# Kernel tuning notes

Measured on AMD Instinct MI355X. Metric: run time of the kernel, lower is better.

Reference implementation:

```python
import jax, jax.numpy as jnp
import numpy as np

EMBED_DIM = 512
NUM_HEADS = 8
HEAD_DIM = EMBED_DIM // NUM_HEADS
GRID_SHAPE = (48, 48)
WINDOW = (16, 16)
BATCH = 2
SEQ = GRID_SHAPE[0] * GRID_SHAPE[1]
NEG = float(np.finfo(np.float16).min)  # matches torch.finfo(torch.float16).min fill


def build_window_mask():
    # replicates: indices = np.indices(grid).flatten(1).T; dist = |i-j|*2; all(dist < window)
    idx = np.indices(GRID_SHAPE).reshape(len(GRID_SHAPE), -1).T  # [N, 2]
    dist = np.abs(idx[:, None, :] - idx[None, :, :]) * 2          # [N, N, 2]
    mask = np.all(dist < np.array(WINDOW)[None, None, :], axis=-1)  # [N, N] bool
    return jnp.asarray(mask)


def setup_inputs() -> dict:
    key = jax.random.key(0)
    ks = jax.random.split(key, 11)
    s = 1.0 / np.sqrt(EMBED_DIM)
    inp = {
        "x_q": jax.random.normal(ks[0], (BATCH, SEQ, EMBED_DIM), jnp.float32),
        "x_k": jax.random.normal(ks[1], (BATCH, SEQ, EMBED_DIM), jnp.float32),
        "x_v": jax.random.normal(ks[2], (BATCH, SEQ, EMBED_DIM), jnp.float32),
        "Wq": jax.random.normal(ks[3], (EMBED_DIM, EMBED_DIM), jnp.float32) * s,
        "bq": jnp.zeros((EMBED_DIM,), jnp.float32),
        "Wk": jax.random.normal(ks[4], (EMBED_DIM, EMBED_DIM), jnp.float32) * s,
        "bk": jnp.zeros((EMBED_DIM,), jnp.float32),
        "Wv": jax.random.normal(ks[5], (EMBED_DIM, EMBED_DIM), jnp.float32) * s,
        "bv": jnp.zeros((EMBED_DIM,), jnp.float32),
        "Wo": jax.random.normal(ks[6], (EMBED_DIM, EMBED_DIM), jnp.float32) * s,
        "bo": jnp.zeros((EMBED_DIM,), jnp.float32),
        "attn_mask": build_window_mask(),
    }
    return inp


def reference(x_q, x_k, x_v, Wq, bq, Wk, bk, Wv, bv, Wo, bo, attn_mask):
    B, S, E = x_q.shape
    H, D = NUM_HEADS, HEAD_DIM

    def proj(x, W, b):
        y = x @ W.T + b                         # [B,S,E]
        return y.reshape(B, S, H, D).transpose(0, 2, 1, 3)  # [B,H,S,D]

    q = proj(x_q, Wq, bq)
    k = proj(x_k, Wk, bk)
    v = proj(x_v, Wv, bv)

    scores = jnp.einsum("bhqd,bhkd->bhqk", q, k) / np.sqrt(D)
    # Windowed branch: per-row gather over allowed keys + softmax == dense
    # softmax with disallowed keys masked to a huge negative value.
    scores = jnp.where(attn_mask[None, None, :, :], scores, NEG)
    probs = jax.nn.softmax(scores, axis=-1)     # dropout=0.0 -> identity
    context = jnp.einsum("bhqk,bhkd->bhqd", probs, v)
    context = context.transpose(0, 2, 1, 3).reshape(B, S, E)
    out = context @ Wo.T + bo
    return out
```

## Files before the change

### kernel.cpp

```cpp
#include <hip/hip_runtime.h>

typedef __attribute__((ext_vector_type(8))) short short8;
typedef __attribute__((ext_vector_type(4))) float f32x4;
typedef __attribute__((ext_vector_type(2))) unsigned int u32x2;
typedef __attribute__((ext_vector_type(4))) unsigned int u32x4;

#define DEV __device__ __forceinline__

#define QH_E 0L
#define KH_E 2359296L
#define VT_E 4718592L
#define CTX_E 7077888L

#define LOG2E 1.4426950408889634f

#define BARRIER() __builtin_amdgcn_s_barrier()
#define SCHED0() __builtin_amdgcn_sched_barrier(0)

DEV unsigned short f2bf(float f) {
  unsigned int x = __float_as_uint(f);
  x = (x + 0x7fffu + ((x >> 16) & 1u)) >> 16;
  return (unsigned short)x;
}

DEV unsigned int pk2(float a, float b) {
  unsigned int r;
  asm("v_cvt_pk_bf16_f32 %0, %1, %2" : "=v"(r) : "v"(a), "v"(b));
  return r;
}

DEV void gl2lds16(const unsigned short* g, unsigned short* l) {
  __builtin_amdgcn_global_load_lds(
      (const __attribute__((address_space(1))) unsigned int*)g,
      (__attribute__((address_space(3))) unsigned int*)l, 16, 0, 0);
}

DEV f32x4 mfma16(short8 a, short8 b, f32x4 c) {
  return __builtin_amdgcn_mfma_f32_16x16x32_bf16(a, b, c, 0, 0, 0);
}

DEV void gemm_qkv(const float* __restrict__ A, const float* __restrict__ W,
                  int m0, int n0, unsigned short* ldsA, unsigned short* ldsB,
                  f32x4 acc[4][2]) {
  const int tid = threadIdx.x;
  const int lane = tid & 63, wvv = tid >> 6;
  const int g = lane >> 4, qi = lane & 15;
  const int wr = wvv >> 1, wc = wvv & 1;
  const int c8 = tid & 7, rbase = tid >> 3;
  const int j8 = (c8 ^ (rbase & 7)) * 8;
  f32x4 ra[4][2];
  f32x4 rw[2][2][2];
#pragma unroll
  for (int mi = 0; mi < 4; ++mi)
#pragma unroll
    for (int ni = 0; ni < 2; ++ni) {
      f32x4 z = {0.f, 0.f, 0.f, 0.f};
      acc[mi][ni] = z;
    }
#define QLA(kt) do {                                                          \
    const int k0_ = (kt) * 64;                                                \
    _Pragma("unroll")                                                         \
    for (int it = 0; it < 4; ++it) {                                          \
      const float* p = A + (long)(m0 + it * 32 + rbase) * 512 + k0_ + j8;     \
      ra[it][0] = *(const f32x4*)p;                                           \
      ra[it][1] = *(const f32x4*)(p + 4);                                     \
    }                                                                         \
  } while (0)
#define QLB(kt) do {                                                          \
    const int k0_ = (kt) * 64;                                                \
    _Pragma("unroll")                                                         \
    for (int it = 0; it < 2; ++it) {                                          \
      const float* p = W + (long)(n0 + it * 32 + rbase) * 512 + k0_ + j8;     \
      rw[(kt) & 1][it][0] = *(const f32x4*)p;                                 \
      rw[(kt) & 1][it][1] = *(const f32x4*)(p + 4);                           \
    }                                                                         \
  } while (0)
#define QWA(bi) do {                                                          \
    _Pragma("unroll")                                                         \
    for (int it = 0; it < 4; ++it) {                                          \
      u32x4 v_;                                                               \
      v_.x = pk2(ra[it][0].x, ra[it][0].y);                                   \
      v_.y = pk2(ra[it][0].z, ra[it][0].w);                                   \
      v_.z = pk2(ra[it][1].x, ra[it][1].y);                                   \
      v_.w = pk2(ra[it][1].z, ra[it][1].w);                                   \
      *(u32x4*)(ldsA + (bi) * 8192 + (it * 256 + tid) * 8) = v_;              \
    }                                                                         \
  } while (0)
#define QWB(bi) do {                                                          \
    _Pragma("unroll")                                                         \
    for (int it = 0; it < 2; ++it) {                                          \
      u32x4 v_;                                                               \
      v_.x = pk2(rw[(bi)][it][0].x, rw[(bi)][it][0].y);                       \
      v_.y = pk2(rw[(bi)][it][0].z, rw[(bi)][it][0].w);                       \
      v_.z = pk2(rw[(bi)][it][1].x, rw[(bi)][it][1].y);                       \
      v_.w = pk2(rw[(bi)][it][1].z, rw[(bi)][it][1].w);                       \
      *(u32x4*)(ldsB + (bi) * 4096 + (it * 256 + tid) * 8) = v_;              \
    }                                                                         \
  } while (0)
  QLA(0); QLB(0); QLB(1);
  QWA(0); QWB(0);
  QLA(1); QLB(2);
  asm volatile("s_waitcnt lgkmcnt(0)" ::: "memory");
  BARRIER();
  SCHED0();
#pragma unroll
  for (int kt = 0; kt < 8; ++kt) {
    const unsigned short* La = ldsA + (kt & 1) * 8192;
    const unsigned short* Lb = ldsB + (kt & 1) * 4096;
    __builtin_amdgcn_s_setprio(1);
#pragma unroll
    for (int kk = 0; kk < 2; ++kk) {
      short8 af[4], bfr[2];
#pragma unroll
      for (int mi = 0; mi < 4; ++mi) {
        int row = 64 * wr + 16 * mi + qi;
        int c16 = (4 * kk + g) ^ (qi & 7);
        af[mi] = *(const short8*)(La + row * 64 + c16 * 8);
      }
#pragma unroll
      for (int ni = 0; ni < 2; ++ni) {
        int row = 32 * wc + 16 * ni + qi;
        int c16 = (4 * kk + g) ^ (qi & 7);
        bfr[ni] = *(const short8*)(Lb + row * 64 + c16 * 8);
      }
#pragma unroll
      for (int mi = 0; mi < 4; ++mi)
#pragma unroll
        for (int ni = 0; ni < 2; ++ni)
          acc[mi][ni] = mfma16(af[mi], bfr[ni], acc[mi][ni]);
    }
    __builtin_amdgcn_s_setprio(0);
    SCHED0();
    if (kt < 7) { QWA((kt + 1) & 1); QWB((kt + 1) & 1); }
    if (kt < 6) QLA(kt + 2);
    if (kt < 5) QLB(kt + 3);
    if (kt < 7) {
      asm volatile("s_waitcnt lgkmcnt(0)" ::: "memory");
      BARRIER();
      SCHED0();
    }
  }
#undef QLA
#undef QLB
#undef QWA
#undef QWB
}

DEV void gemm_o(const unsigned short* __restrict__ A, const float* __restrict__ W,
                int m0, int n0, unsigned short* ldsA, unsigned short* ldsB,
                f32x4 acc[2][2]) {
  const int tid = threadIdx.x;
  const int lane = tid & 63, wvv = tid >> 6;
  const int g = lane >> 4, qi = lane & 15;
  const int wr = wvv >> 1, wc = wvv & 1;
  const int c8 = tid & 7, rbase = tid >> 3;
  const int j8 = (c8 ^ (rbase & 7)) * 8;
  u32x4 rab[2][2];
  f32x4 rw[2][2][2];
#pragma unroll
  for (int mi = 0; mi < 2; ++mi)
#pragma unroll
    for (int ni = 0; ni < 2; ++ni) {
      f32x4 z = {0.f, 0.f, 0.f, 0.f};
      acc[mi][ni] = z;
    }
#define OLA(kt) do {                                                          \
    const int k0_ = (kt) * 64;                                                \
    _Pragma("unroll")                                                         \
    for (int it = 0; it < 2; ++it)                                            \
      rab[(kt) & 1][it] =                                                     \
          *(const u32x4*)(A + (long)(m0 + it * 32 + rbase) * 512 + k0_ + j8); \
  } while (0)
#define OLB(kt) do {                                                          \
    const int k0_ = (kt) * 64;                                                \
    _Pragma("unroll")                                                         \
    for (int it = 0; it < 2; ++it) {                                          \
      const float* p = W + (long)(n0 + it * 32 + rbase) * 512 + k0_ + j8;     \
      rw[(kt) & 1][it][0] = *(const f32x4*)p;                                 \
// ... 33 lines not shown
    for (int kk = 0; kk < 2; ++kk) {
      short8 af[2], bfr[2];
#pragma unroll
      for (int mi = 0; mi < 2; ++mi) {
        int row = 32 * wr + 16 * mi + qi;
        int c16 = (4 * kk + g) ^ (qi & 7);
        af[mi] = *(const short8*)(La + row * 64 + c16 * 8);
      }
#pragma unroll
      for (int ni = 0; ni < 2; ++ni) {
        int row = 32 * wc + 16 * ni + qi;
        int c16 = (4 * kk + g) ^ (qi & 7);
        bfr[ni] = *(const short8*)(Lb + row * 64 + c16 * 8);
      }
#pragma unroll
      for (int mi = 0; mi < 2; ++mi)
#pragma unroll
        for (int ni = 0; ni < 2; ++ni)
          acc[mi][ni] = mfma16(af[mi], bfr[ni], acc[mi][ni]);
    }
    __builtin_amdgcn_s_setprio(0);
    SCHED0();
    if (kt < 6) OW(kt + 2);
    if (kt < 4) { OLA(kt + 4); OLB(kt + 4); }
    if (kt < 7) {
      asm volatile("s_waitcnt lgkmcnt(0)" ::: "memory");
      BARRIER();
      SCHED0();
    }
  }
#undef OLA
#undef OLB
#undef OW
}

__global__ __launch_bounds__(256, 3) void proj_qkv_kernel(
    const float* __restrict__ xq, const float* __restrict__ xk,
    const float* __restrict__ xv, const float* __restrict__ wqp,
    const float* __restrict__ wkp, const float* __restrict__ wvp,
    const float* __restrict__ bq, const float* __restrict__ bk,
    const float* __restrict__ bv, unsigned short* __restrict__ ws) {
  __shared__ unsigned short ldsA[2 * 8192];
  __shared__ unsigned short ldsB[2 * 4096];
  int f = blockIdx.x;
  int wid = (f & 7) * 108 + (f >> 3);
  const int z = wid / 288;
  const int rem = wid % 288;
  const int m0 = (rem >> 3) * 128, n0 = (rem & 7) * 64;
  const float *A, *W, *bias;
  unsigned short* dst;
  float oscale;
  int mode;
  if (z == 0)      { A = xq; W = wqp; bias = bq; oscale = 0.125f * LOG2E; dst = ws + QH_E; mode = 0; }
  else if (z == 1) { A = xk; W = wkp; bias = bk; oscale = 1.0f;           dst = ws + KH_E; mode = 0; }
  else             { A = xv; W = wvp; bias = bv; oscale = 1.0f;           dst = ws + VT_E; mode = 1; }
  f32x4 acc[4][2];
  gemm_qkv(A, W, m0, n0, ldsA, ldsB, acc);
  const int lane = threadIdx.x & 63, wvv = threadIdx.x >> 6;
  const int g = lane >> 4, qi = lane & 15;
  const int wr = wvv >> 1, wc = wvv & 1;
#pragma unroll
  for (int ni = 0; ni < 2; ++ni) {
    int n = n0 + 32 * wc + 16 * ni + qi;
    float bb = bias[n];
    int h = n >> 6, d = n & 63;
#pragma unroll
    for (int mi = 0; mi < 4; ++mi) {
      int m = m0 + 64 * wr + 16 * mi + 4 * g;
      int b = (m >= 2304) ? 1 : 0;
      int s = m - b * 2304;
      if (mode == 0) {
#pragma unroll
        for (int r = 0; r < 4; ++r) {
          float v = (acc[mi][ni][r] + bb) * oscale;
          dst[((long)((b * 8 + h) * 2304 + s + r)) * 64 + d] = f2bf(v);
        }
      } else {
        u32x2 o;
        o.x = pk2(acc[mi][ni][0] + bb, acc[mi][ni][1] + bb);
        o.y = pk2(acc[mi][ni][2] + bb, acc[mi][ni][3] + bb);
        *(u32x2*)(dst + ((long)((b * 8 + h) * 64 + d)) * 2304 + s) = o;
      }
    }
  }
}

__global__ __launch_bounds__(256, 3) void proj_out_kernel(
    const unsigned short* __restrict__ ws, const float* __restrict__ wop,
    const float* __restrict__ bo, float* __restrict__ out) {
  __shared__ unsigned short ldsA[3 * 4096];
  __shared__ unsigned short ldsB[3 * 4096];
  int f = blockIdx.x;
  int wid = (f & 7) * 72 + (f >> 3);
  const int m0 = (wid >> 3) * 64, n0 = (wid & 7) * 64;
  f32x4 acc[2][2];
  gemm_o(ws + CTX_E, wop, m0, n0, ldsA, ldsB, acc);
  const int lane = threadIdx.x & 63, wvv = threadIdx.x >> 6;
  const int g = lane >> 4, qi = lane & 15;
  const int wr = wvv >> 1, wc = wvv & 1;
#pragma unroll
  for (int ni = 0; ni < 2; ++ni) {
    int n = n0 + 32 * wc + 16 * ni + qi;
    float bb = bo[n];
#pragma unroll
    for (int mi = 0; mi < 2; ++mi) {
#pragma unroll
      for (int r = 0; r < 4; ++r) {
        int m = m0 + 32 * wr + 16 * mi + 4 * g + r;
        out[(long)m * 512 + n] = acc[mi][ni][r] + bb;
      }
    }
  }
}

__global__ __launch_bounds__(192) void attn_kernel(unsigned short* __restrict__ ws) {
  __shared__ unsigned short ldsKV[3 * 7168];
  __shared__ unsigned short ldsP[3][16][72];
  __shared__ unsigned short ldsDum[512];
  const int tid = threadIdx.x;
  const int lane = tid & 63, wv = tid >> 6;
  const int g = lane >> 4, qi = lane & 15;
  int f = blockIdx.x;
  int wid = (f & 7) * 96 + (f >> 3);
  const int bh = wid / 48, r = wid - 48 * bh;
  const int ci = wv * 16 + qi;
  const unsigned short* Kh = ws + KH_E + (long)bh * 2304 * 64;
  const unsigned short* Vt = ws + VT_E + (long)bh * 64 * 2304;
  const int q = r * 48 + ci;
  const unsigned short* qp = ws + QH_E + ((long)bh * 2304 + q) * 64;
  f32x4 qraw0 = *(const f32x4*)(qp + 8 * g);
  f32x4 qraw1 = *(const f32x4*)(qp + 32 + 8 * g);
  asm volatile("" : "+v"(qraw0), "+v"(qraw1));
  short8 qf0 = __builtin_bit_cast(short8, qraw0);
  short8 qf1 = __builtin_bit_cast(short8, qraw1);
  float msk[12];
#pragma unroll
  for (int mb = 0; mb < 3; ++mb)
#pragma unroll
    for (int rr = 0; rr < 4; ++rr) {
      int cj = 16 * mb + 4 * g + rr;
      msk[mb * 4 + rr] = ((unsigned)(ci - cj + 7) <= 14u) ? 0.f : -1e30f;
    }
  {
    u32x2 z2; z2.x = 0u; z2.y = 0u;
    *(u32x2*)(&ldsP[wv][qi][48 + 4 * g]) = z2;
  }
  f32x4 cacc[4];
#pragma unroll
  for (int mb = 0; mb < 4; ++mb) { f32x4 z = {0.f, 0.f, 0.f, 0.f}; cacc[mb] = z; }
  float lrun = 0.f;

#define ASTAGE(bi, rj) do {                                                   \
    unsigned short* Lb_ = ldsKV + (bi) * 7168;                                \
    const unsigned short* Ks_ = Kh + (long)(rj) * 3072;                       \
    _Pragma("unroll")                                                         \
    for (int it = 0; it < 5; ++it) {                                          \
      int u = it * 192 + tid;                                                 \
      if (u < 384) {                                                          \
        int kr = u >> 3, c = u & 7, cs = c ^ (kr & 7);                        \
        gl2lds16(Ks_ + kr * 64 + cs * 8, Lb_ + u * 8);                        \
      } else if (u < 896) {                                                   \
        int v2 = u - 384;                                                     \
        int d = v2 >> 3, c = v2 & 7, cs = c ^ (d & 7);                        \
        long jb = (long)(rj) * 48 + cs * 8;                                   \
        if (jb > 2296) jb = 2296;                                             \
        gl2lds16(Vt + (long)d * 2304 + jb, Lb_ + u * 8);                      \
      } else {                                                                \
        gl2lds16(Kh + (u - 896) * 8, ldsDum + (u - 896) * 8);                 \
      }                                                                       \
    }                                                                         \
  } while (0)

  const int rlo = (r > 7) ? r - 7 : 0;
  const int rhi = (r < 40) ? r + 7 : 47;
  const int nch = rhi - rlo + 1;
  ASTAGE(0, rlo);
  ASTAGE(1, rlo + 1);
  for (int t = 0; t < nch; ++t) {
    if (t + 1 < nch) { asm volatile("s_waitcnt vmcnt(5)" ::: "memory"); }
    else             { asm volatile("s_waitcnt vmcnt(0)" ::: "memory"); }
    BARRIER();
    SCHED0();
    if (t + 2 < nch) ASTAGE((t + 2) % 3, rlo + t + 2);
    const unsigned short* Kt = ldsKV + (t % 3) * 7168;
    const unsigned short* Vm = Kt + 3072;
    f32x4 sacc[3];
#pragma unroll
    for (int mb = 0; mb < 3; ++mb) { f32x4 z = {0.f, 0.f, 0.f, 0.f}; sacc[mb] = z; }
    __builtin_amdgcn_s_setprio(1);
#pragma unroll
    for (int kk = 0; kk < 2; ++kk) {
      short8 qf = kk ? qf1 : qf0;
#pragma unroll
      for (int mb = 0; mb < 3; ++mb) {
        int row = 16 * mb + qi;
        int c16 = (4 * kk + g) ^ (qi & 7);
        short8 ka = *(const short8*)(Kt + row * 64 + c16 * 8);
        sacc[mb] = mfma16(ka, qf, sacc[mb]);
      }
    }
    __builtin_amdgcn_s_setprio(0);
    unsigned int pw[6];
#pragma unroll
    for (int mb = 0; mb < 3; ++mb) {
      float p0 = __builtin_amdgcn_exp2f(sacc[mb][0] + msk[mb * 4 + 0]);
      float p1 = __builtin_amdgcn_exp2f(sacc[mb][1] + msk[mb * 4 + 1]);
      float p2 = __builtin_amdgcn_exp2f(sacc[mb][2] + msk[mb * 4 + 2]);
      float p3 = __builtin_amdgcn_exp2f(sacc[mb][3] + msk[mb * 4 + 3]);
      lrun += (p0 + p1) + (p2 + p3);
      pw[2 * mb] = pk2(p0, p1);
      pw[2 * mb + 1] = pk2(p2, p3);
    }
#pragma unroll
    for (int mb = 0; mb < 3; ++mb) {
      u32x2 pv2; pv2.x = pw[2 * mb]; pv2.y = pw[2 * mb + 1];
      *(u32x2*)(&ldsP[wv][qi][16 * mb + 4 * g]) = pv2;
    }
    __builtin_amdgcn_s_setprio(1);
#pragma unroll
    for (int kk = 0; kk < 2; ++kk) {
      short8 pb = *(const short8*)(&ldsP[wv][qi][32 * kk + 8 * g]);
#pragma unroll
      for (int mb = 0; mb < 4; ++mb) {
        int row = 16 * mb + qi;
        int c16 = (4 * kk + g) ^ (qi & 7);
        short8 va = *(const short8*)(Vm + row * 64 + c16 * 8);
        cacc[mb] = mfma16(va, pb, cacc[mb]);
      }
    }
    __builtin_amdgcn_s_setprio(0);
  }
#undef ASTAGE
  lrun += __shfl_xor(lrun, 16);
  lrun += __shfl_xor(lrun, 32);
  const float inv = 1.0f / lrun;
  unsigned short* ctx = ws + CTX_E;
  const int b2 = bh >> 3, h2 = bh & 7;
#pragma unroll
  for (int mb = 0; mb < 4; ++mb) {
    u32x2 o;
    o.x = pk2(cacc[mb][0] * inv, cacc[mb][1] * inv);
    o.y = pk2(cacc[mb][2] * inv, cacc[mb][3] * inv);
    long off = ((long)(b2 * 2304 + q)) * 512 + h2 * 64 + 16 * mb + 4 * g;
    *(u32x2*)(ctx + off) = o;
  }
}

extern "C" void kernel_launch(void* const* d_in, const int* in_sizes, int n_in,
                              void* d_out, int out_size, void* d_ws, size_t ws_size,
                              hipStream_t stream) {
  const float* xq = (const float*)d_in[0];
  const float* xk = (const float*)d_in[1];
  const float* xv = (const float*)d_in[2];
  const float* wq = (const float*)d_in[3];
  const float* bq = (const float*)d_in[4];
  const float* wk = (const float*)d_in[5];
  const float* bk = (const float*)d_in[6];
  const float* wv = (const float*)d_in[7];
  const float* bv = (const float*)d_in[8];
  const float* wo = (const float*)d_in[9];
  const float* bo = (const float*)d_in[10];
  unsigned short* ws = (unsigned short*)d_ws;
  float* out = (float*)d_out;

  proj_qkv_kernel<<<dim3(864), dim3(256), 0, stream>>>(xq, xk, xv, wq, wk, wv,
                                                       bq, bk, bv, ws);
  attn_kernel<<<dim3(768), dim3(192), 0, stream>>>(ws);
  proj_out_kernel<<<dim3(576), dim3(256), 0, stream>>>(ws, wo, bo, out);
}
```

Measured before the change: 57.49 us.

## Software-pipeline QK of next chunk with softmax-PV of current chunk

Restructures the windowed attention loop so the QK^T MFMAs for chunk t+1 are issued before the exp/softmax and PV MFMAs of chunk t, using two ping-pong score register sets and a manually unrolled by-two loop. The aim is to overlap the matrix-core work with the transcendental and LDS work so dependent latencies are hidden. The trade-off is more live registers, a stricter vmcnt(0) wait before each stage where the old code used vmcnt(5), and more complex buffer rotation. This could reduce occupancy or expose load latency.

New measurement: 57.90 us. No clear change (+0.7%).

```diff
diff --git a/kernel.cpp b/kernel.cpp
--- a/kernel.cpp
+++ b/kernel.cpp
@@ -382,77 +382,102 @@
     }                                                                         \
   } while (0)
 
+#define AQK(KB, S) do {                                                       \
+    const unsigned short* Kt_ = (KB);                                         \
+    _Pragma("unroll")                                                         \
+    for (int mb = 0; mb < 3; ++mb) { f32x4 z = {0.f,0.f,0.f,0.f}; S[mb] = z; }\
+    __builtin_amdgcn_s_setprio(1);                                            \
+    _Pragma("unroll")                                                         \
+    for (int kk = 0; kk < 2; ++kk) {                                          \
+      short8 qf_ = kk ? qf1 : qf0;                                            \
+      _Pragma("unroll")                                                       \
+      for (int mb = 0; mb < 3; ++mb) {                                        \
+        int row = 16 * mb + qi;                                               \
+        int c16 = (4 * kk + g) ^ (qi & 7);                                    \
+        short8 ka = *(const short8*)(Kt_ + row * 64 + c16 * 8);               \
+        S[mb] = mfma16(ka, qf_, S[mb]);                                       \
+      }                                                                       \
+    }                                                                         \
+    __builtin_amdgcn_s_setprio(0);                                            \
+  } while (0)
+
+#define ASMPV(VB, S) do {                                                     \
+    const unsigned short* Vm_ = (VB);                                         \
+    unsigned int pw[6];                                                       \
+    _Pragma("unroll")                                                         \
+    for (int mb = 0; mb < 3; ++mb) {                                          \
+      float p0 = __builtin_amdgcn_exp2f(S[mb][0] + msk[mb * 4 + 0]);          \
+      float p1 = __builtin_amdgcn_exp2f(S[mb][1] + msk[mb * 4 + 1]);          \
+      float p2 = __builtin_amdgcn_exp2f(S[mb][2] + msk[mb * 4 + 2]);          \
+      float p3 = __builtin_amdgcn_exp2f(S[mb][3] + msk[mb * 4 + 3]);          \
+      lrun += (p0 + p1) + (p2 + p3);                                          \
+      pw[2 * mb] = pk2(p0, p1);                                               \
+      pw[2 * mb + 1] = pk2(p2, p3);                                           \
+    }                                                                         \
+    _Pragma("unroll")                                                         \
+    for (int mb = 0; mb < 3; ++mb) {                                          \
+      u32x2 pv2; pv2.x = pw[2 * mb]; pv2.y = pw[2 * mb + 1];                  \
+      *(u32x2*)(&ldsP[wv][qi][16 * mb + 4 * g]) = pv2;                        \
+    }                                                                         \
+    __builtin_amdgcn_s_setprio(1);                                            \
+    _Pragma("unroll")                                                         \
+    for (int kk = 0; kk < 2; ++kk) {                                          \
+      short8 pb = *(const short8*)(&ldsP[wv][qi][32 * kk + 8 * g]);           \
+      _Pragma("unroll")                                                       \
+      for (int mb = 0; mb < 4; ++mb) {                                        \
+        int row = 16 * mb + qi;                                               \
+        int c16 = (4 * kk + g) ^ (qi & 7);                                    \
+        short8 va = *(const short8*)(Vm_ + row * 64 + c16 * 8);               \
+        cacc[mb] = mfma16(va, pb, cacc[mb]);                                  \
+      }                                                                       \
+    }                                                                         \
+    __builtin_amdgcn_s_setprio(0);                                            \
+  } while (0)
+
   const int rlo = (r > 7) ? r - 7 : 0;
   const int rhi = (r < 40) ? r + 7 : 47;
   const int nch = rhi - rlo + 1;
+  f32x4 sE[3], sO[3];
   ASTAGE(0, rlo);
   ASTAGE(1, rlo + 1);
-  for (int t = 0; t < nch; ++t) {
-    if (t + 1 < nch) { asm volatile("s_waitcnt vmcnt(5)" ::: "memory"); }
-    else             { asm volatile("s_waitcnt vmcnt(0)" ::: "memory"); }
+  asm volatile("s_waitcnt vmcnt(5)" ::: "memory");
+  BARRIER();
+  SCHED0();
+  AQK(ldsKV, sE);
+  int bc = 0;
+  for (int t = 0; t < nch; t += 2) {
+    const int b1 = (bc + 1 == 3) ? 0 : bc + 1;
+    const int b2 = (b1 + 1 == 3) ? 0 : b1 + 1;
+    asm volatile("s_waitcnt vmcnt(0)" ::: "memory");
     BARRIER();
     SCHED0();
-    if (t + 2 < nch) ASTAGE((t + 2) % 3, rlo + t + 2);
-    const unsigned short* Kt = ldsKV + (t % 3) * 7168;
-    const unsigned short* Vm = Kt + 3072;
-    f32x4 sacc[3];
-#pragma unroll
-    for (int mb = 0; mb < 3; ++mb) { f32x4 z = {0.f, 0.f, 0.f, 0.f}; sacc[mb] = z; }
-    __builtin_amdgcn_s_setprio(1);
-#pragma unroll
-    for (int kk = 0; kk < 2; ++kk) {
-      short8 qf = kk ? qf1 : qf0;
-#pragma unroll
-      for (int mb = 0; mb < 3; ++mb) {
-        int row = 16 * mb + qi;
-        int c16 = (4 * kk + g) ^ (qi & 7);
-        short8 ka = *(const short8*)(Kt + row * 64 + c16 * 8);
-        sacc[mb] = mfma16(ka, qf, sacc[mb]);
-      }
-    }
-    __builtin_amdgcn_s_setprio(0);
-    unsigned int pw[6];
-#pragma unroll
-    for (int mb = 0; mb < 3; ++mb) {
-      float p0 = __builtin_amdgcn_exp2f(sacc[mb][0] + msk[mb * 4 + 0]);
-      float p1 = __builtin_amdgcn_exp2f(sacc[mb][1] + msk[mb * 4 + 1]);
-      float p2 = __builtin_amdgcn_exp2f(sacc[mb][2] + msk[mb * 4 + 2]);
-      float p3 = __builtin_amdgcn_exp2f(sacc[mb][3] + msk[mb * 4 + 3]);
-      lrun += (p0 + p1) + (p2 + p3);
-      pw[2 * mb] = pk2(p0, p1);
-      pw[2 * mb + 1] = pk2(p2, p3);
-    }
-#pragma unroll
-    for (int mb = 0; mb < 3; ++mb) {
-      u32x2 pv2; pv2.x = pw[2 * mb]; pv2.y = pw[2 * mb + 1];
-      *(u32x2*)(&ldsP[wv][qi][16 * mb + 4 * g]) = pv2;
-    }
-    __builtin_amdgcn_s_setprio(1);
-#pragma unroll
-    for (int kk = 0; kk < 2; ++kk) {
-      short8 pb = *(const short8*)(&ldsP[wv][qi][32 * kk + 8 * g]);
-#pragma unroll
-      for (int mb = 0; mb < 4; ++mb) {
-        int row = 16 * mb + qi;
-        int c16 = (4 * kk + g) ^ (qi & 7);
-        short8 va = *(const short8*)(Vm + row * 64 + c16 * 8);
-        cacc[mb] = mfma16(va, pb, cacc[mb]);
-      }
-    }
-    __builtin_amdgcn_s_setprio(0);
+    if (t + 2 < nch) ASTAGE(b2, rlo + t + 2);
+    if (t + 1 < nch) AQK(ldsKV + b1 * 7168, sO);
+    ASMPV(ldsKV + bc * 7168 + 3072, sE);
+    if (t + 1 < nch) {
+      asm volatile("s_waitcnt vmcnt(0)" ::: "memory");
+      BARRIER();
+      SCHED0();
+      if (t + 3 < nch) ASTAGE(bc, rlo + t + 3);
+      if (t + 2 < nch) AQK(ldsKV + b2 * 7168, sE);
+      ASMPV(ldsKV + b1 * 7168 + 3072, sO);
+    }
+    bc = b2;
   }
 #undef ASTAGE
+#undef AQK
+#undef ASMPV
   lrun += __shfl_xor(lrun, 16);
   lrun += __shfl_xor(lrun, 32);
   const float inv = 1.0f / lrun;
   unsigned short* ctx = ws + CTX_E;
-  const int b2 = bh >> 3, h2 = bh & 7;
+  const int b2w = bh >> 3, h2 = bh & 7;
 #pragma unroll
   for (int mb = 0; mb < 4; ++mb) {
     u32x2 o;
     o.x = pk2(cacc[mb][0] * inv, cacc[mb][1] * inv);
     o.y = pk2(cacc[mb][2] * inv, cacc[mb][3] * inv);
-    long off = ((long)(b2 * 2304 + q)) * 512 + h2 * 64 + 16 * mb + 4 * g;
+    long off = ((long)(b2w * 2304 + q)) * 512 + h2 * 64 + 16 * mb + 4 * g;
     *(u32x2*)(ctx + off) = o;
   }
 }
```

## Enlarge QKV projection tiles and share K/V staging across two query rows

Applied to the files above, without the earlier changes.

The QKV projection kernel now uses 512-thread blocks with 128x128 output tiles instead of 256-thread 128x64 tiles, halving the block count and raising reuse of each loaded A tile. The attention kernel now processes two adjacent query grid rows per 384-thread block, so each staged K/V row chunk in LDS serves both rows. Chunks outside a row's window are skipped per wave. This cuts redundant global K/V traffic, but gives fewer blocks, a larger LDS footprint and some idle waves at window edges.

Measured after the change: 61.67 us. +7.3%, slower.

```diff
diff --git a/kernel.cpp b/kernel.cpp
--- a/kernel.cpp
+++ b/kernel.cpp
@@ -39,74 +39,94 @@
   return __builtin_amdgcn_mfma_f32_16x16x32_bf16(a, b, c, 0, 0, 0);
 }
 
-DEV void gemm_qkv(const float* __restrict__ A, const float* __restrict__ W,
-                  int m0, int n0, unsigned short* ldsA, unsigned short* ldsB,
-                  f32x4 acc[4][2]) {
+__global__ __launch_bounds__(512, 4) void proj_qkv_kernel(
+    const float* __restrict__ xq, const float* __restrict__ xk,
+    const float* __restrict__ xv, const float* __restrict__ wqp,
+    const float* __restrict__ wkp, const float* __restrict__ wvp,
+    const float* __restrict__ bq, const float* __restrict__ bk,
+    const float* __restrict__ bv, unsigned short* __restrict__ ws) {
+  __shared__ unsigned short ldsA[2 * 8192];
+  __shared__ unsigned short ldsB[2 * 8192];
+  int f = blockIdx.x;
+  int wid = (f & 7) * 54 + (f >> 3);
+  const int z = wid / 144;
+  const int rem = wid % 144;
+  const int m0 = (rem >> 2) * 128, n0 = (rem & 3) * 128;
+  const float *A, *W, *bias;
+  unsigned short* dst;
+  float oscale;
+  int mode;
+  if (z == 0)      { A = xq; W = wqp; bias = bq; oscale = 0.125f * LOG2E; dst = ws + QH_E; mode = 0; }
+  else if (z == 1) { A = xk; W = wkp; bias = bk; oscale = 1.0f;           dst = ws + KH_E; mode = 0; }
+  else             { A = xv; W = wvp; bias = bv; oscale = 1.0f;           dst = ws + VT_E; mode = 1; }
   const int tid = threadIdx.x;
   const int lane = tid & 63, wvv = tid >> 6;
   const int g = lane >> 4, qi = lane & 15;
-  const int wr = wvv >> 1, wc = wvv & 1;
+  const int wr = wvv >> 2, wc = wvv & 3;
   const int c8 = tid & 7, rbase = tid >> 3;
-  const int j8 = (c8 ^ (rbase & 7)) * 8;
-  f32x4 ra[4][2];
-  f32x4 rw[2][2][2];
+  f32x4 ra[2][2], rw[2][2];
+  f32x4 acc[4][2];
 #pragma unroll
   for (int mi = 0; mi < 4; ++mi)
 #pragma unroll
     for (int ni = 0; ni < 2; ++ni) {
-      f32x4 z = {0.f, 0.f, 0.f, 0.f};
-      acc[mi][ni] = z;
-    }
-#define QLA(kt) do {                                                          \
+      f32x4 z4 = {0.f, 0.f, 0.f, 0.f};
+      acc[mi][ni] = z4;
+    }
+#define PLA(kt) do {                                                          \
     const int k0_ = (kt) * 64;                                                \
     _Pragma("unroll")                                                         \
-    for (int it = 0; it < 4; ++it) {                                          \
-      const float* p = A + (long)(m0 + it * 32 + rbase) * 512 + k0_ + j8;     \
+    for (int it = 0; it < 2; ++it) {                                          \
+      int row = it * 64 + rbase;                                              \
+      int cs = c8 ^ (row & 7);                                                \
+      const float* p = A + (long)(m0 + row) * 512 + k0_ + cs * 8;             \
       ra[it][0] = *(const f32x4*)p;                                           \
       ra[it][1] = *(const f32x4*)(p + 4);                                     \
     }                                                                         \
   } while (0)
-#define QLB(kt) do {                                                          \
+#define PLB(kt) do {                                                          \
     const int k0_ = (kt) * 64;                                                \
     _Pragma("unroll")                                                         \
     for (int it = 0; it < 2; ++it) {                                          \
-      const float* p = W + (long)(n0 + it * 32 + rbase) * 512 + k0_ + j8;     \
-      rw[(kt) & 1][it][0] = *(const f32x4*)p;                                 \
-      rw[(kt) & 1][it][1] = *(const f32x4*)(p + 4);                           \
-    }                                                                         \
-  } while (0)
-#define QWA(bi) do {                                                          \
-    _Pragma("unroll")                                                         \
-    for (int it = 0; it < 4; ++it) {                                          \
+      int row = it * 64 + rbase;                                              \
+      int cs = c8 ^ (row & 7);                                                \
+      const float* p = W + (long)(n0 + row) * 512 + k0_ + cs * 8;             \
+      rw[it][0] = *(const f32x4*)p;                                           \
+      rw[it][1] = *(const f32x4*)(p + 4);                                     \
+    }                                                                         \
+  } while (0)
+#define PWA(bi) do {                                                          \
+    _Pragma("unroll")                                                         \
+    for (int it = 0; it < 2; ++it) {                                          \
       u32x4 v_;                                                               \
       v_.x = pk2(ra[it][0].x, ra[it][0].y);                                   \
       v_.y = pk2(ra[it][0].z, ra[it][0].w);                                   \
       v_.z = pk2(ra[it][1].x, ra[it][1].y);                                   \
       v_.w = pk2(ra[it][1].z, ra[it][1].w);                                   \
-      *(u32x4*)(ldsA + (bi) * 8192 + (it * 256 + tid) * 8) = v_;              \
-    }                                                                         \
-  } while (0)
-#define QWB(bi) do {                                                          \
+      *(u32x4*)(ldsA + (bi) * 8192 + (it * 512 + tid) * 8) = v_;              \
+    }                                                                         \
+  } while (0)
+#define PWB(bi) do {                                                          \
     _Pragma("unroll")                                                         \
     for (int it = 0; it < 2; ++it) {                                          \
       u32x4 v_;                                                               \
-      v_.x = pk2(rw[(bi)][it][0].x, rw[(bi)][it][0].y);                       \
-      v_.y = pk2(rw[(bi)][it][0].z, rw[(bi)][it][0].w);                       \
-      v_.z = pk2(rw[(bi)][it][1].x, rw[(bi)][it][1].y);                       \
-      v_.w = pk2(rw[(bi)][it][1].z, rw[(bi)][it][1].w);                       \
-      *(u32x4*)(ldsB + (bi) * 4096 + (it * 256 + tid) * 8) = v_;              \
-    }                                                                         \
-  } while (0)
-  QLA(0); QLB(0); QLB(1);
-  QWA(0); QWB(0);
-  QLA(1); QLB(2);
+      v_.x = pk2(rw[it][0].x, rw[it][0].y);                                   \
+      v_.y = pk2(rw[it][0].z, rw[it][0].w);                                   \
+      v_.z = pk2(rw[it][1].x, rw[it][1].y);                                   \
+      v_.w = pk2(rw[it][1].z, rw[it][1].w);                                   \
+      *(u32x4*)(ldsB + (bi) * 8192 + (it * 512 + tid) * 8) = v_;              \
+    }                                                                         \
+  } while (0)
+  PLA(0); PLB(0);
+  PWA(0); PWB(0);
+  PLA(1); PLB(1);
   asm volatile("s_waitcnt lgkmcnt(0)" ::: "memory");
   BARRIER();
   SCHED0();
 #pragma unroll
   for (int kt = 0; kt < 8; ++kt) {
     const unsigned short* La = ldsA + (kt & 1) * 8192;
-    const unsigned short* Lb = ldsB + (kt & 1) * 4096;
+    const unsigned short* Lb = ldsB + (kt & 1) * 8192;
     __builtin_amdgcn_s_setprio(1);
 #pragma unroll
     for (int kk = 0; kk < 2; ++kk) {
@@ -131,19 +151,42 @@
     }
     __builtin_amdgcn_s_setprio(0);
     SCHED0();
-    if (kt < 7) { QWA((kt + 1) & 1); QWB((kt + 1) & 1); }
-    if (kt < 6) QLA(kt + 2);
-    if (kt < 5) QLB(kt + 3);
+    if (kt < 7) { PWA((kt + 1) & 1); PWB((kt + 1) & 1); }
+    if (kt < 6) { PLA(kt + 2); PLB(kt + 2); }
     if (kt < 7) {
       asm volatile("s_waitcnt lgkmcnt(0)" ::: "memory");
       BARRIER();
       SCHED0();
     }
   }
-#undef QLA
-#undef QLB
-#undef QWA
-#undef QWB
+#undef PLA
+#undef PLB
+#undef PWA
+#undef PWB
+#pragma unroll
+  for (int ni = 0; ni < 2; ++ni) {
+    int n = n0 + 32 * wc + 16 * ni + qi;
+    float bb = bias[n];
+    int h = n >> 6, d = n & 63;
+#pragma unroll
+    for (int mi = 0; mi < 4; ++mi) {
+      int m = m0 + 64 * wr + 16 * mi + 4 * g;
+      int b = (m >= 2304) ? 1 : 0;
+      int s = m - b * 2304;
+      if (mode == 0) {
+#pragma unroll
+        for (int r = 0; r < 4; ++r) {
+          float v = (acc[mi][ni][r] + bb) * oscale;
+          dst[((long)((b * 8 + h) * 2304 + s + r)) * 64 + d] = f2bf(v);
+        }
+      } else {
+        u32x2 o;
+        o.x = pk2(acc[mi][ni][0] + bb, acc[mi][ni][1] + bb);
+        o.y = pk2(acc[mi][ni][2] + bb, acc[mi][ni][3] + bb);
+        *(u32x2*)(dst + ((long)((b * 8 + h) * 64 + d)) * 2304 + s) = o;
+      }
+    }
+  }
 }
 
 DEV void gemm_o(const unsigned short* __restrict__ A, const float* __restrict__ W,
@@ -243,57 +286,6 @@
 #undef OLA
 #undef OLB
 #undef OW
-}
-
-__global__ __launch_bounds__(256, 3) void proj_qkv_kernel(
-    const float* __restrict__ xq, const float* __restrict__ xk,
-    const float* __restrict__ xv, const float* __restrict__ wqp,
-    const float* __restrict__ wkp, const float* __restrict__ wvp,
-    const float* __restrict__ bq, const float* __restrict__ bk,
-    const float* __restrict__ bv, unsigned short* __restrict__ ws) {
-  __shared__ unsigned short ldsA[2 * 8192];
-  __shared__ unsigned short ldsB[2 * 4096];
-  int f = blockIdx.x;
-  int wid = (f & 7) * 108 + (f >> 3);
-  const int z = wid / 288;
-  const int rem = wid % 288;
-  const int m0 = (rem >> 3) * 128, n0 = (rem & 7) * 64;
-  const float *A, *W, *bias;
-  unsigned short* dst;
-  float oscale;
-  int mode;
-  if (z == 0)      { A = xq; W = wqp; bias = bq; oscale = 0.125f * LOG2E; dst = ws + QH_E; mode = 0; }
-  else if (z == 1) { A = xk; W = wkp; bias = bk; oscale = 1.0f;           dst = ws + KH_E; mode = 0; }
-  else             { A = xv; W = wvp; bias = bv; oscale = 1.0f;           dst = ws + VT_E; mode = 1; }
-  f32x4 acc[4][2];
-  gemm_qkv(A, W, m0, n0, ldsA, ldsB, acc);
-  const int lane = threadIdx.x & 63, wvv = threadIdx.x >> 6;
-  const int g = lane >> 4, qi = lane & 15;
-  const int wr = wvv >> 1, wc = wvv & 1;
-#pragma unroll
-  for (int ni = 0; ni < 2; ++ni) {
-    int n = n0 + 32 * wc + 16 * ni + qi;
-    float bb = bias[n];
-    int h = n >> 6, d = n & 63;
-#pragma unroll
-    for (int mi = 0; mi < 4; ++mi) {
-      int m = m0 + 64 * wr + 16 * mi + 4 * g;
-      int b = (m >= 2304) ? 1 : 0;
-      int s = m - b * 2304;
-      if (mode == 0) {
-#pragma unroll
-        for (int r = 0; r < 4; ++r) {
-          float v = (acc[mi][ni][r] + bb) * oscale;
-          dst[((long)((b * 8 + h) * 2304 + s + r)) * 64 + d] = f2bf(v);
-        }
-      } else {
-        u32x2 o;
-        o.x = pk2(acc[mi][ni][0] + bb, acc[mi][ni][1] + bb);
-        o.y = pk2(acc[mi][ni][2] + bb, acc[mi][ni][3] + bb);
-        *(u32x2*)(dst + ((long)((b * 8 + h) * 64 + d)) * 2304 + s) = o;
-      }
-    }
-  }
 }
 
 __global__ __launch_bounds__(256, 3) void proj_out_kernel(
@@ -324,20 +316,24 @@
   }
 }
 
-__global__ __launch_bounds__(192) void attn_kernel(unsigned short* __restrict__ ws) {
+__global__ __launch_bounds__(384) void attn_kernel(unsigned short* __restrict__ ws) {
   __shared__ unsigned short ldsKV[3 * 7168];
-  __shared__ unsigned short ldsP[3][16][72];
+  __shared__ unsigned short ldsP[6][16][72];
   __shared__ unsigned short ldsDum[512];
   const int tid = threadIdx.x;
   const int lane = tid & 63, wv = tid >> 6;
   const int g = lane >> 4, qi = lane & 15;
   int f = blockIdx.x;
-  int wid = (f & 7) * 96 + (f >> 3);
-  const int bh = wid / 48, r = wid - 48 * bh;
-  const int ci = wv * 16 + qi;
+  int wid = (f & 7) * 48 + (f >> 3);
+  const int bh = wid / 24, p = wid - 24 * bh;
+  const int r0 = 2 * p;
+  const int half = (wv >= 3) ? 1 : 0;
+  const int cw = wv - 3 * half;
+  const int ri = r0 + half;
+  const int ci = cw * 16 + qi;
   const unsigned short* Kh = ws + KH_E + (long)bh * 2304 * 64;
   const unsigned short* Vt = ws + VT_E + (long)bh * 64 * 2304;
-  const int q = r * 48 + ci;
+  const int q = ri * 48 + ci;
   const unsigned short* qp = ws + QH_E + ((long)bh * 2304 + q) * 64;
   f32x4 qraw0 = *(const f32x4*)(qp + 8 * g);
   f32x4 qraw1 = *(const f32x4*)(qp + 32 + 8 * g);
@@ -365,8 +361,8 @@
     unsigned short* Lb_ = ldsKV + (bi) * 7168;                                \
     const unsigned short* Ks_ = Kh + (long)(rj) * 3072;                       \
     _Pragma("unroll")                                                         \
-    for (int it = 0; it < 5; ++it) {                                          \
-      int u = it * 192 + tid;                                                 \
+    for (int it = 0; it < 3; ++it) {                                          \
+      int u = it * 384 + tid;                                                 \
       if (u < 384) {                                                          \
         int kr = u >> 3, c = u & 7, cs = c ^ (kr & 7);                        \
         gl2lds16(Ks_ + kr * 64 + cs * 8, Lb_ + u * 8);                        \
@@ -377,82 +373,85 @@
         if (jb > 2296) jb = 2296;                                             \
         gl2lds16(Vt + (long)d * 2304 + jb, Lb_ + u * 8);                      \
       } else {                                                                \
-        gl2lds16(Kh + (u - 896) * 8, ldsDum + (u - 896) * 8);                 \
+        gl2lds16(Kh + ((u - 896) & 63) * 8, ldsDum + ((u - 896) & 63) * 8);   \
       }                                                                       \
     }                                                                         \
   } while (0)
 
-  const int rlo = (r > 7) ? r - 7 : 0;
-  const int rhi = (r < 40) ? r + 7 : 47;
+  const int rlo = (r0 > 7) ? r0 - 7 : 0;
+  const int rhi = (r0 + 8 < 47) ? r0 + 8 : 47;
   const int nch = rhi - rlo + 1;
   ASTAGE(0, rlo);
   ASTAGE(1, rlo + 1);
   for (int t = 0; t < nch; ++t) {
-    if (t + 1 < nch) { asm volatile("s_waitcnt vmcnt(5)" ::: "memory"); }
+    if (t + 1 < nch) { asm volatile("s_waitcnt vmcnt(3)" ::: "memory"); }
     else             { asm volatile("s_waitcnt vmcnt(0)" ::: "memory"); }
     BARRIER();
     SCHED0();
     if (t + 2 < nch) ASTAGE((t + 2) % 3, rlo + t + 2);
-    const unsigned short* Kt = ldsKV + (t % 3) * 7168;
-    const unsigned short* Vm = Kt + 3072;
-    f32x4 sacc[3];
-#pragma unroll
-    for (int mb = 0; mb < 3; ++mb) { f32x4 z = {0.f, 0.f, 0.f, 0.f}; sacc[mb] = z; }
-    __builtin_amdgcn_s_setprio(1);
-#pragma unroll
-    for (int kk = 0; kk < 2; ++kk) {
-      short8 qf = kk ? qf1 : qf0;
+    const int rj = rlo + t;
+    if ((unsigned)(ri - rj + 7) <= 14u) {
+      const unsigned short* Kt = ldsKV + (t % 3) * 7168;
+      const unsigned short* Vm = Kt + 3072;
+      f32x4 sacc[3];
+#pragma unroll
+      for (int mb = 0; mb < 3; ++mb) { f32x4 z = {0.f, 0.f, 0.f, 0.f}; sacc[mb] = z; }
+      __builtin_amdgcn_s_setprio(1);
+#pragma unroll
+      for (int kk = 0; kk < 2; ++kk) {
+        short8 qf_ = kk ? qf1 : qf0;
+#pragma unroll
+        for (int mb = 0; mb < 3; ++mb) {
+          int row = 16 * mb + qi;
+          int c16 = (4 * kk + g) ^ (qi & 7);
+          short8 ka = *(const short8*)(Kt + row * 64 + c16 * 8);
+          sacc[mb] = mfma16(ka, qf_, sacc[mb]);
+        }
+      }
+      __builtin_amdgcn_s_setprio(0);
+      unsigned int pw[6];
 #pragma unroll
       for (int mb = 0; mb < 3; ++mb) {
-        int row = 16 * mb + qi;
-        int c16 = (4 * kk + g) ^ (qi & 7);
-        short8 ka = *(const short8*)(Kt + row * 64 + c16 * 8);
-        sacc[mb] = mfma16(ka, qf, sacc[mb]);
-      }
-    }
-    __builtin_amdgcn_s_setprio(0);
-    unsigned int pw[6];
-#pragma unroll
-    for (int mb = 0; mb < 3; ++mb) {
-      float p0 = __builtin_amdgcn_exp2f(sacc[mb][0] + msk[mb * 4 + 0]);
-      float p1 = __builtin_amdgcn_exp2f(sacc[mb][1] + msk[mb * 4 + 1]);
-      float p2 = __builtin_amdgcn_exp2f(sacc[mb][2] + msk[mb * 4 + 2]);
-      float p3 = __builtin_amdgcn_exp2f(sacc[mb][3] + msk[mb * 4 + 3]);
-      lrun += (p0 + p1) + (p2 + p3);
-      pw[2 * mb] = pk2(p0, p1);
-      pw[2 * mb + 1] = pk2(p2, p3);
-    }
-#pragma unroll
-    for (int mb = 0; mb < 3; ++mb) {
-      u32x2 pv2; pv2.x = pw[2 * mb]; pv2.y = pw[2 * mb + 1];
-      *(u32x2*)(&ldsP[wv][qi][16 * mb + 4 * g]) = pv2;
-    }
-    __builtin_amdgcn_s_setprio(1);
-#pragma unroll
-    for (int kk = 0; kk < 2; ++kk) {
-      short8 pb = *(const short8*)(&ldsP[wv][qi][32 * kk + 8 * g]);
-#pragma unroll
-      for (int mb = 0; mb < 4; ++mb) {
-        int row = 16 * mb + qi;
-        int c16 = (4 * kk + g) ^ (qi & 7);
-        short8 va = *(const short8*)(Vm + row * 64 + c16 * 8);
-        cacc[mb] = mfma16(va, pb, cacc[mb]);
-      }
-    }
-    __builtin_amdgcn_s_setprio(0);
+        float p0 = __builtin_amdgcn_exp2f(sacc[mb][0] + msk[mb * 4 + 0]);
+        float p1 = __builtin_amdgcn_exp2f(sacc[mb][1] + msk[mb * 4 + 1]);
+        float p2 = __builtin_amdgcn_exp2f(sacc[mb][2] + msk[mb * 4 + 2]);
+        float p3 = __builtin_amdgcn_exp2f(sacc[mb][3] + msk[mb * 4 + 3]);
+        lrun += (p0 + p1) + (p2 + p3);
+        pw[2 * mb] = pk2(p0, p1);
+        pw[2 * mb + 1] = pk2(p2, p3);
+      }
+#pragma unroll
+      for (int mb = 0; mb < 3; ++mb) {
+        u32x2 pv2; pv2.x = pw[2 * mb]; pv2.y = pw[2 * mb + 1];
+        *(u32x2*)(&ldsP[wv][qi][16 * mb + 4 * g]) = pv2;
+      }
+      __builtin_amdgcn_s_setprio(1);
+#pragma unroll
+      for (int kk = 0; kk < 2; ++kk) {
+        short8 pb = *(const short8*)(&ldsP[wv][qi][32 * kk + 8 * g]);
+#pragma unroll
+        for (int mb = 0; mb < 4; ++mb) {
+          int row = 16 * mb + qi;
+          int c16 = (4 * kk + g) ^ (qi & 7);
+          short8 va = *(const short8*)(Vm + row * 64 + c16 * 8);
+          cacc[mb] = mfma16(va, pb, cacc[mb]);
+        }
+      }
+      __builtin_amdgcn_s_setprio(0);
+    }
   }
 #undef ASTAGE
   lrun += __shfl_xor(lrun, 16);
   lrun += __shfl_xor(lrun, 32);
   const float inv = 1.0f / lrun;
   unsigned short* ctx = ws + CTX_E;
-  const int b2 = bh >> 3, h2 = bh & 7;
+  const int b2w = bh >> 3, h2 = bh & 7;
 #pragma unroll
   for (int mb = 0; mb < 4; ++mb) {
     u32x2 o;
     o.x = pk2(cacc[mb][0] * inv, cacc[mb][1] * inv);
     o.y = pk2(cacc[mb][2] * inv, cacc[mb][3] * inv);
-    long off = ((long)(b2 * 2304 + q)) * 512 + h2 * 64 + 16 * mb + 4 * g;
+    long off = ((long)(b2w * 2304 + q)) * 512 + h2 * 64 + 16 * mb + 4 * g;
     *(u32x2*)(ctx + off) = o;
   }
 }
@@ -474,8 +473,8 @@
   unsigned short* ws = (unsigned short*)d_ws;
   float* out = (float*)d_out;
 
-  proj_qkv_kernel<<<dim3(864), dim3(256), 0, stream>>>(xq, xk, xv, wq, wk, wv,
+  proj_qkv_kernel<<<dim3(432), dim3(512), 0, stream>>>(xq, xk, xv, wq, wk, wv,
                                                        bq, bk, bv, ws);
-  attn_kernel<<<dim3(768), dim3(192), 0, stream>>>(ws);
+  attn_kernel<<<dim3(384), dim3(384), 0, stream>>>(ws);
   proj_out_kernel<<<dim3(576), dim3(256), 0, stream>>>(ws, wo, bo, out);
 }
```

## Pre-convert QKV inputs to bf16 and use direct global-to-LDS loads in projection

Applied to the files above, without the earlier changes.

Adds a separate conversion kernel that casts x_q/x_k/x_v and the three weight matrices to bf16 in workspace, folding the softmax scale into Wq. The QKV projection then loads bf16 tiles straight into LDS with global_load_lds and a three-stage buffer, using 128x128 tiles with 512 threads instead of converting fp32 in registers. This removes the register staging and conversion from the GEMM loop but adds an extra kernel launch and a full fp32-read, bf16-write pass over the inputs. The bias is now scaled before adding instead of the sum being scaled, which is equivalent up to rounding.

Result: slower. 60.56 us (+5.3%).

```diff
diff --git a/kernel.cpp b/kernel.cpp
--- a/kernel.cpp
+++ b/kernel.cpp
@@ -7,10 +7,16 @@
 
 #define DEV __device__ __forceinline__
 
-#define QH_E 0L
-#define KH_E 2359296L
-#define VT_E 4718592L
-#define CTX_E 7077888L
+#define XQ_E 0L
+#define XK_E 2359296L
+#define XV_E 4718592L
+#define WQ_E 7077888L
+#define WK_E 7340032L
+#define WV_E 7602176L
+#define QH_E 7864320L
+#define KH_E 10223616L
+#define VT_E 12582912L
+#define CTX_E 14942208L
 
 #define LOG2E 1.4426950408889634f
 
@@ -39,111 +45,121 @@
   return __builtin_amdgcn_mfma_f32_16x16x32_bf16(a, b, c, 0, 0, 0);
 }
 
-DEV void gemm_qkv(const float* __restrict__ A, const float* __restrict__ W,
-                  int m0, int n0, unsigned short* ldsA, unsigned short* ldsB,
-                  f32x4 acc[4][2]) {
+__global__ __launch_bounds__(256) void cvt_kernel(
+    const float* __restrict__ xq, const float* __restrict__ xk,
+    const float* __restrict__ xv, const float* __restrict__ wq,
+    const float* __restrict__ wk, const float* __restrict__ wv,
+    unsigned short* __restrict__ ws) {
+  int t = blockIdx.x * 256 + threadIdx.x;
+  const float* src;
+  long rel, dstE;
+  float sc = 1.0f;
+  if (t < 1769472) {
+    if (t < 589824)       { src = xq; rel = t;            dstE = XQ_E; }
+    else if (t < 1179648) { src = xk; rel = t - 589824;   dstE = XK_E; }
+    else                  { src = xv; rel = t - 1179648;  dstE = XV_E; }
+  } else {
+    int u = t - 1769472;
+    if (u < 65536)        { src = wq; rel = u;            dstE = WQ_E; sc = 0.125f * LOG2E; }
+    else if (u < 131072)  { src = wk; rel = u - 65536;    dstE = WK_E; }
+    else                  { src = wv; rel = u - 131072;   dstE = WV_E; }
+  }
+  f32x4 v = *(const f32x4*)(src + rel * 4);
+  v *= sc;
+  u32x2 o;
+  o.x = pk2(v.x, v.y);
+  o.y = pk2(v.z, v.w);
+  *(u32x2*)(ws + dstE + rel * 4) = o;
+}
+
+__global__ __launch_bounds__(512, 6) void proj_qkv_kernel(
+    unsigned short* __restrict__ ws, const float* __restrict__ bq,
+    const float* __restrict__ bk, const float* __restrict__ bv) {
+  __shared__ unsigned short ldsA[3 * 4096];
+  __shared__ unsigned short ldsB[3 * 4096];
+  int f = blockIdx.x;
+  int wid = (f & 7) * 54 + (f >> 3);
+  const int z = wid / 144;
+  const int rem = wid % 144;
+  const int m0 = (rem >> 2) * 128, n0 = (rem & 3) * 128;
+  const unsigned short *A, *W;
+  const float* bias;
+  unsigned short* dst;
+  float bscale;
+  int mode;
+  if (z == 0)      { A = ws + XQ_E; W = ws + WQ_E; bias = bq; bscale = 0.125f * LOG2E; dst = ws + QH_E; mode = 0; }
+  else if (z == 1) { A = ws + XK_E; W = ws + WK_E; bias = bk; bscale = 1.0f;           dst = ws + KH_E; mode = 0; }
+  else             { A = ws + XV_E; W = ws + WV_E; bias = bv; bscale = 1.0f;           dst = ws + VT_E; mode = 1; }
   const int tid = threadIdx.x;
   const int lane = tid & 63, wvv = tid >> 6;
   const int g = lane >> 4, qi = lane & 15;
-  const int wr = wvv >> 1, wc = wvv & 1;
-  const int c8 = tid & 7, rbase = tid >> 3;
-  const int j8 = (c8 ^ (rbase & 7)) * 8;
-  f32x4 ra[4][2];
-  f32x4 rw[2][2][2];
+  const int wr = wvv >> 2, wc = wvv & 3;
+  const int srow = tid >> 2, sc8 = tid & 3;
+  f32x4 acc[4][2];
 #pragma unroll
   for (int mi = 0; mi < 4; ++mi)
 #pragma unroll
     for (int ni = 0; ni < 2; ++ni) {
-      f32x4 z = {0.f, 0.f, 0.f, 0.f};
-      acc[mi][ni] = z;
-    }
-#define QLA(kt) do {                                                          \
-    const int k0_ = (kt) * 64;                                                \
-    _Pragma("unroll")                                                         \
-    for (int it = 0; it < 4; ++it) {                                          \
-      const float* p = A + (long)(m0 + it * 32 + rbase) * 512 + k0_ + j8;     \
-      ra[it][0] = *(const f32x4*)p;                                           \
-      ra[it][1] = *(const f32x4*)(p + 4);                                     \
-    }                                                                         \
+      f32x4 z4 = {0.f, 0.f, 0.f, 0.f};
+      acc[mi][ni] = z4;
+    }
+#define STG(bi, kt) do {                                                      \
+    const long k0_ = (long)(kt) * 32 + sc8 * 8;                               \
+    gl2lds16(A + (long)(m0 + srow) * 512 + k0_, ldsA + (bi) * 4096 + tid * 8);\
+    gl2lds16(W + (long)(n0 + srow) * 512 + k0_, ldsB + (bi) * 4096 + tid * 8);\
   } while (0)
-#define QLB(kt) do {                                                          \
-    const int k0_ = (kt) * 64;                                                \
-    _Pragma("unroll")                                                         \
-    for (int it = 0; it < 2; ++it) {                                          \
-      const float* p = W + (long)(n0 + it * 32 + rbase) * 512 + k0_ + j8;     \
-      rw[(kt) & 1][it][0] = *(const f32x4*)p;                                 \
-      rw[(kt) & 1][it][1] = *(const f32x4*)(p + 4);                           \
-    }                                                                         \
-  } while (0)
-#define QWA(bi) do {                                                          \
-    _Pragma("unroll")                                                         \
-    for (int it = 0; it < 4; ++it) {                                          \
-      u32x4 v_;                                                               \
-      v_.x = pk2(ra[it][0].x, ra[it][0].y);                                   \
-      v_.y = pk2(ra[it][0].z, ra[it][0].w);                                   \
-      v_.z = pk2(ra[it][1].x, ra[it][1].y);                                   \
-      v_.w = pk2(ra[it][1].z, ra[it][1].w);                                   \
-      *(u32x4*)(ldsA + (bi) * 8192 + (it * 256 + tid) * 8) = v_;              \
-    }                                                                         \
-  } while (0)
-#define QWB(bi) do {                                                          \
-    _Pragma("unroll")                                                         \
-    for (int it = 0; it < 2; ++it) {                                          \
-      u32x4 v_;                                                               \
-      v_.x = pk2(rw[(bi)][it][0].x, rw[(bi)][it][0].y);                       \
-      v_.y = pk2(rw[(bi)][it][0].z, rw[(bi)][it][0].w);                       \
-      v_.z = pk2(rw[(bi)][it][1].x, rw[(bi)][it][1].y);                       \
-      v_.w = pk2(rw[(bi)][it][1].z, rw[(bi)][it][1].w);                       \
-      *(u32x4*)(ldsB + (bi) * 4096 + (it * 256 + tid) * 8) = v_;              \
-    }                                                                         \
-  } while (0)
-  QLA(0); QLB(0); QLB(1);
-  QWA(0); QWB(0);
-  QLA(1); QLB(2);
-  asm volatile("s_waitcnt lgkmcnt(0)" ::: "memory");
-  BARRIER();
-  SCHED0();
-#pragma unroll
-  for (int kt = 0; kt < 8; ++kt) {
-    const unsigned short* La = ldsA + (kt & 1) * 8192;
-    const unsigned short* Lb = ldsB + (kt & 1) * 4096;
+  STG(0, 0);
+  STG(1, 1);
+#pragma unroll
+  for (int t = 0; t < 16; ++t) {
+    if (t < 15) { asm volatile("s_waitcnt vmcnt(2)" ::: "memory"); }
+    else        { asm volatile("s_waitcnt vmcnt(0)" ::: "memory"); }
+    BARRIER();
+    SCHED0();
+    if (t + 2 < 16) STG((t + 2) % 3, t + 2);
+    const unsigned short* La = ldsA + (t % 3) * 4096;
+    const unsigned short* Lb = ldsB + (t % 3) * 4096;
     __builtin_amdgcn_s_setprio(1);
-#pragma unroll
-    for (int kk = 0; kk < 2; ++kk) {
-      short8 af[4], bfr[2];
-#pragma unroll
-      for (int mi = 0; mi < 4; ++mi) {
-        int row = 64 * wr + 16 * mi + qi;
-        int c16 = (4 * kk + g) ^ (qi & 7);
-        af[mi] = *(const short8*)(La + row * 64 + c16 * 8);
-      }
-#pragma unroll
-      for (int ni = 0; ni < 2; ++ni) {
-        int row = 32 * wc + 16 * ni + qi;
-        int c16 = (4 * kk + g) ^ (qi & 7);
-        bfr[ni] = *(const short8*)(Lb + row * 64 + c16 * 8);
-      }
-#pragma unroll
-      for (int mi = 0; mi < 4; ++mi)
-#pragma unroll
-        for (int ni = 0; ni < 2; ++ni)
-          acc[mi][ni] = mfma16(af[mi], bfr[ni], acc[mi][ni]);
-    }
+    short8 af[4], bfr[2];
+#pragma unroll
+    for (int mi = 0; mi < 4; ++mi)
+      af[mi] = *(const short8*)(La + (64 * wr + 16 * mi + qi) * 32 + g * 8);
+#pragma unroll
+    for (int ni = 0; ni < 2; ++ni)
+      bfr[ni] = *(const short8*)(Lb + (32 * wc + 16 * ni + qi) * 32 + g * 8);
+#pragma unroll
+    for (int mi = 0; mi < 4; ++mi)
+#pragma unroll
+      for (int ni = 0; ni < 2; ++ni)
+        acc[mi][ni] = mfma16(af[mi], bfr[ni], acc[mi][ni]);
     __builtin_amdgcn_s_setprio(0);
     SCHED0();
-    if (kt < 7) { QWA((kt + 1) & 1); QWB((kt + 1) & 1); }
-    if (kt < 6) QLA(kt + 2);
-    if (kt < 5) QLB(kt + 3);
-    if (kt < 7) {
-      asm volatile("s_waitcnt lgkmcnt(0)" ::: "memory");
-      BARRIER();
-      SCHED0();
-    }
-  }
-#undef QLA
-#undef QLB
-#undef QWA
-#undef QWB
+  }
+#undef STG
+#pragma unroll
+  for (int ni = 0; ni < 2; ++ni) {
+    int n = n0 + 32 * wc + 16 * ni + qi;
+    float bb = bias[n] * bscale;
+    int h = n >> 6, d = n & 63;
+#pragma unroll
+    for (int mi = 0; mi < 4; ++mi) {
+      int m = m0 + 64 * wr + 16 * mi + 4 * g;
+      int b = (m >= 2304) ? 1 : 0;
+      int s = m - b * 2304;
+      if (mode == 0) {
+#pragma unroll
+        for (int r = 0; r < 4; ++r) {
+          float v = acc[mi][ni][r] + bb;
+          dst[((long)((b * 8 + h) * 2304 + s + r)) * 64 + d] = f2bf(v);
+        }
+      } else {
+        u32x2 o;
+        o.x = pk2(acc[mi][ni][0] + bb, acc[mi][ni][1] + bb);
+        o.y = pk2(acc[mi][ni][2] + bb, acc[mi][ni][3] + bb);
+        *(u32x2*)(dst + ((long)((b * 8 + h) * 64 + d)) * 2304 + s) = o;
+      }
+    }
+  }
 }
 
 DEV void gemm_o(const unsigned short* __restrict__ A, const float* __restrict__ W,
@@ -245,57 +261,6 @@
 #undef OW
 }
 
-__global__ __launch_bounds__(256, 3) void proj_qkv_kernel(
-    const float* __restrict__ xq, const float* __restrict__ xk,
-    const float* __restrict__ xv, const float* __restrict__ wqp,
-    const float* __restrict__ wkp, const float* __restrict__ wvp,
-    const float* __restrict__ bq, const float* __restrict__ bk,
-    const float* __restrict__ bv, unsigned short* __restrict__ ws) {
-  __shared__ unsigned short ldsA[2 * 8192];
-  __shared__ unsigned short ldsB[2 * 4096];
-  int f = blockIdx.x;
-  int wid = (f & 7) * 108 + (f >> 3);
-  const int z = wid / 288;
-  const int rem = wid % 288;
-  const int m0 = (rem >> 3) * 128, n0 = (rem & 7) * 64;
-  const float *A, *W, *bias;
-  unsigned short* dst;
-  float oscale;
-  int mode;
-  if (z == 0)      { A = xq; W = wqp; bias = bq; oscale = 0.125f * LOG2E; dst = ws + QH_E; mode = 0; }
-  else if (z == 1) { A = xk; W = wkp; bias = bk; oscale = 1.0f;           dst = ws + KH_E; mode = 0; }
-  else             { A = xv; W = wvp; bias = bv; oscale = 1.0f;           dst = ws + VT_E; mode = 1; }
-  f32x4 acc[4][2];
-  gemm_qkv(A, W, m0, n0, ldsA, ldsB, acc);
-  const int lane = threadIdx.x & 63, wvv = threadIdx.x >> 6;
-  const int g = lane >> 4, qi = lane & 15;
-  const int wr = wvv >> 1, wc = wvv & 1;
-#pragma unroll
-  for (int ni = 0; ni < 2; ++ni) {
-    int n = n0 + 32 * wc + 16 * ni + qi;
-    float bb = bias[n];
-    int h = n >> 6, d = n & 63;
-#pragma unroll
-    for (int mi = 0; mi < 4; ++mi) {
-      int m = m0 + 64 * wr + 16 * mi + 4 * g;
-      int b = (m >= 2304) ? 1 : 0;
-      int s = m - b * 2304;
-      if (mode == 0) {
-#pragma unroll
-        for (int r = 0; r < 4; ++r) {
-          float v = (acc[mi][ni][r] + bb) * oscale;
-          dst[((long)((b * 8 + h) * 2304 + s + r)) * 64 + d] = f2bf(v);
-        }
-      } else {
-        u32x2 o;
-        o.x = pk2(acc[mi][ni][0] + bb, acc[mi][ni][1] + bb);
-        o.y = pk2(acc[mi][ni][2] + bb, acc[mi][ni][3] + bb);
-        *(u32x2*)(dst + ((long)((b * 8 + h) * 64 + d)) * 2304 + s) = o;
-      }
-    }
-  }
-}
-
 __global__ __launch_bounds__(256, 3) void proj_out_kernel(
     const unsigned short* __restrict__ ws, const float* __restrict__ wop,
     const float* __restrict__ bo, float* __restrict__ out) {
@@ -401,13 +366,13 @@
     __builtin_amdgcn_s_setprio(1);
 #pragma unroll
     for (int kk = 0; kk < 2; ++kk) {
-      short8 qf = kk ? qf1 : qf0;
+      short8 qf_ = kk ? qf1 : qf0;
 #pragma unroll
       for (int mb = 0; mb < 3; ++mb) {
         int row = 16 * mb + qi;
         int c16 = (4 * kk + g) ^ (qi & 7);
         short8 ka = *(const short8*)(Kt + row * 64 + c16 * 8);
-        sacc[mb] = mfma16(ka, qf, sacc[mb]);
+        sacc[mb] = mfma16(ka, qf_, sacc[mb]);
       }
     }
     __builtin_amdgcn_s_setprio(0);
@@ -446,13 +411,13 @@
   lrun += __shfl_xor(lrun, 32);
   const float inv = 1.0f / lrun;
   unsigned short* ctx = ws + CTX_E;
-  const int b2 = bh >> 3, h2 = bh & 7;
+  const int b2w = bh >> 3, h2 = bh & 7;
 #pragma unroll
   for (int mb = 0; mb < 4; ++mb) {
     u32x2 o;
     o.x = pk2(cacc[mb][0] * inv, cacc[mb][1] * inv);
     o.y = pk2(cacc[mb][2] * inv, cacc[mb][3] * inv);
-    long off = ((long)(b2 * 2304 + q)) * 512 + h2 * 64 + 16 * mb + 4 * g;
+    long off = ((long)(b2w * 2304 + q)) * 512 + h2 * 64 + 16 * mb + 4 * g;
     *(u32x2*)(ctx + off) = o;
   }
 }
@@ -474,8 +439,8 @@
   unsigned short* ws = (unsigned short*)d_ws;
   float* out = (float*)d_out;
 
-  proj_qkv_kernel<<<dim3(864), dim3(256), 0, stream>>>(xq, xk, xv, wq, wk, wv,
-                                                       bq, bk, bv, ws);
+  cvt_kernel<<<dim3(7680), dim3(256), 0, stream>>>(xq, xk, xv, wq, wk, wv, ws);
+  proj_qkv_kernel<<<dim3(432), dim3(512), 0, stream>>>(ws, bq, bk, bv);
   attn_kernel<<<dim3(768), dim3(192), 0, stream>>>(ws);
   proj_out_kernel<<<dim3(576), dim3(256), 0, stream>>>(ws, wo, bo, out);
 }
```
